# Performance work log

Hardware: AMD Instinct MI355X
Metric: run time of the kernel (lower is better)

Reference implementation:

```python
import jax, jax.numpy as jnp
import numpy as np

N = 64    # input_size (number of causal nodes)
H = 512   # hidden_size
M = 64    # mediate_size
B = 1024  # batched derivative evaluations (original processes one (1,N) state at a time)


def setup_inputs() -> dict:
    key = jax.random.key(0)
    ks = jax.random.split(key, 8)
    s = lambda fan_in: 1.0 / np.sqrt(fan_in)
    x = jax.random.normal(ks[0], (B, N), dtype=jnp.float32)
    # stacked per-node weights (one set per node i in 0..N-1)
    W1 = jax.random.uniform(ks[1], (N, H, N), jnp.float32, -s(N), s(N))        # net_1 layer 1, no bias
    W2 = jax.random.uniform(ks[2], (N, M, H), jnp.float32, -s(H), s(H))        # net_1 layer 2, no bias
    W3 = jax.random.uniform(ks[3], (N, H, M + N), jnp.float32, -s(M + N), s(M + N))  # net_3 layer 1
    b3 = jax.random.uniform(ks[4], (N, H), jnp.float32, -s(M + N), s(M + N))
    W4 = jax.random.uniform(ks[5], (N, H), jnp.float32, -s(H), s(H))           # net_3 layer 2 (out dim 1)
    b4 = jax.random.uniform(ks[6], (N,), jnp.float32, -s(H), s(H))
    return {"x": x, "W1": W1, "W2": W2, "W3": W3, "b3": b3, "W4": W4, "b4": b4}


def reference(x, W1, W2, W3, b3, W4, b4):
    # Faithful DAG-case CausalDerivative.forward, batched over B states and
    # grouped over the N per-node MLPs (replacing N python-loop iterations).
    eye = jnp.eye(N, dtype=x.dtype)
    inputs_1 = x[:, None, :] * (1.0 - eye)          # (B, N, N): node i sees all-but-own value
    inputs_2 = x[:, None, :] * eye                  # (B, N, N): node i sees only own value
    h1 = jax.nn.relu(jnp.einsum('bni,nhi->bnh', inputs_1, W1))   # (B, N, H)
    r1 = jax.nn.relu(jnp.einsum('bnh,nmh->bnm', h1, W2))         # (B, N, M)
    rep3 = jnp.concatenate([r1, inputs_2], axis=-1)              # (B, N, M+N)
    h3 = jax.nn.relu(jnp.einsum('bnk,nhk->bnh', rep3, W3) + b3)  # (B, N, H)
    out = jax.nn.relu(jnp.einsum('bnh,nh->bn', h3, W4) + b4)     # (B, N) derivatives
    return out
```

## Files before the change

kernel.cpp:

```cpp
#include <hip/hip_runtime.h>

#define NN 64
#define HH 512

typedef _Float16 h8 __attribute__((ext_vector_type(8)));
typedef float    fx4 __attribute__((ext_vector_type(4)));

#define MFMA __builtin_amdgcn_mfma_f32_16x16x32_f16

__device__ __forceinline__ void cvt_store16(_Float16* d, const float4* p) {
    h8 h0, h1;
    h0[0]=(_Float16)p[0].x; h0[1]=(_Float16)p[0].y; h0[2]=(_Float16)p[0].z; h0[3]=(_Float16)p[0].w;
    h0[4]=(_Float16)p[1].x; h0[5]=(_Float16)p[1].y; h0[6]=(_Float16)p[1].z; h0[7]=(_Float16)p[1].w;
    h1[0]=(_Float16)p[2].x; h1[1]=(_Float16)p[2].y; h1[2]=(_Float16)p[2].z; h1[3]=(_Float16)p[2].w;
    h1[4]=(_Float16)p[3].x; h1[5]=(_Float16)p[3].y; h1[6]=(_Float16)p[3].z; h1[7]=(_Float16)p[3].w;
    *(h8*)d = h0; *((h8*)d + 1) = h1;
}

__global__ __launch_bounds__(256, 2)
void causal_mfma3(const float* __restrict__ x,  const float* __restrict__ W1,
                  const float* __restrict__ W2, const float* __restrict__ W3,
                  const float* __restrict__ b3, const float* __restrict__ W4,
                  const float* __restrict__ b4, float* __restrict__ out)
{
    __shared__ __align__(16) char smem[61952];
    _Float16* W1c  = (_Float16*)smem;
    _Float16* W2c  = W1c + 2 * 4608;
    _Float16* priv = W2c + 2 * 4608;
    float*    w3cs = (float*)(smem + 55296);
    float*    b3s  = w3cs + 512;
    float*    w4s  = b3s + 512;
    float*    xns  = w4s + 512;

    const int tid  = threadIdx.x;
    const int bid  = blockIdx.x;
    const int n    = bid & 63;
    const int tile = bid >> 6;
    const int lane = tid & 63;
    const int pos  = lane & 15;
    const int quad = lane >> 4;
    const int wv   = __builtin_amdgcn_readfirstlane(tid >> 6);
    const int row0 = tile * 128;
    const int wrow = wv << 5;

    const float* W1n = W1 + (size_t)n * HH * NN;
    const float* W2n = W2 + (size_t)n * NN * HH;
    const float* W3n = W3 + (size_t)n * HH * 128;

    const int trow = tid >> 2;
    const int tcol = (tid & 3) << 4;

    {
        float4 p1[4], p2[4];
        #pragma unroll
        for (int q = 0; q < 4; ++q) p1[q] = *(const float4*)(W1n + trow * 64 + tcol + q * 4);
        #pragma unroll
        for (int q = 0; q < 4; ++q) p2[q] = *(const float4*)(W2n + (size_t)trow * HH + tcol + q * 4);
        #pragma unroll
        for (int k = 0; k < 2; ++k) {
            const int h = tid + k * 256;
            w3cs[h] = W3n[(size_t)h * 128 + 64 + n];
            b3s[h]  = b3[n * HH + h];
            w4s[h]  = W4[n * HH + h];
        }
        if (tid < 128) xns[tid] = x[(size_t)(row0 + tid) * NN + n];
        cvt_store16(W1c + trow * 72 + tcol, p1);
        cvt_store16(W2c + trow * 72 + tcol, p2);
    }

    h8 aX[2][2];
    #pragma unroll
    for (int mt = 0; mt < 2; ++mt)
        #pragma unroll
        for (int ks = 0; ks < 2; ++ks) {
            const float* p = x + (size_t)(row0 + wrow + mt * 16 + pos) * NN + ks * 32 + quad * 8;
            float4 a = *(const float4*)p, bq = *(const float4*)(p + 4);
            float v[8] = {a.x, a.y, a.z, a.w, bq.x, bq.y, bq.z, bq.w};
            const int base = ks * 32 + quad * 8;
            #pragma unroll
            for (int j = 0; j < 8; ++j) if (base + j == n) v[j] = 0.f;
            h8 h;
            #pragma unroll
            for (int j = 0; j < 8; ++j) h[j] = (_Float16)v[j];
            aX[mt][ks] = h;
        }
    __syncthreads();

    _Float16* P = priv + wv * 2304;

    fx4 acc2[2][4] = {};
    for (int c = 0; c < 8; ++c) {
        const int cb = c & 1;
        float4 p1[4], p2[4];
        if (c < 7) {
            const int hb1 = (c + 1) << 6;
            #pragma unroll
            for (int q = 0; q < 4; ++q) p1[q] = *(const float4*)(W1n + (hb1 + trow) * 64 + tcol + q * 4);
            #pragma unroll
            for (int q = 0; q < 4; ++q) p2[q] = *(const float4*)(W2n + (size_t)trow * HH + hb1 + tcol + q * 4);
        }
        const _Float16* W1L = W1c + cb * 4608;
        fx4 accA[2][4] = {};
        #pragma unroll
        for (int ks = 0; ks < 2; ++ks)
            #pragma unroll
            for (int nt = 0; nt < 4; ++nt) {
                h8 bf = *(const h8*)(W1L + (nt * 16 + pos) * 72 + ks * 32 + quad * 8);
                accA[0][nt] = MFMA(aX[0][ks], bf, accA[0][nt], 0, 0, 0);
                accA[1][nt] = MFMA(aX[1][ks], bf, accA[1][nt], 0, 0, 0);
            }
        #pragma unroll
        for (int mt = 0; mt < 2; ++mt)
            #pragma unroll
            for (int nt = 0; nt < 4; ++nt)
                #pragma unroll
                for (int r = 0; r < 4; ++r)
                    P[(mt * 16 + quad * 4 + r) * 72 + nt * 16 + pos] =
                        (_Float16)fmaxf(accA[mt][nt][r], 0.f);
        h8 aH[2][2];
        #pragma unroll
        for (int mt = 0; mt < 2; ++mt)
            #pragma unroll
            for (int ks = 0; ks < 2; ++ks)
                aH[mt][ks] = *(const h8*)(P + (mt * 16 + pos) * 72 + ks * 32 + quad * 8);
        const _Float16* W2L = W2c + cb * 4608;
        #pragma unroll
        for (int ks = 0; ks < 2; ++ks)
            #pragma unroll
            for (int cm = 0; cm < 4; ++cm) {
                h8 bf = *(const h8*)(W2L + (cm * 16 + pos) * 72 + ks * 32 + quad * 8);
                acc2[0][cm] = MFMA(aH[0][ks], bf, acc2[0][cm], 0, 0, 0);
                acc2[1][cm] = MFMA(aH[1][ks], bf, acc2[1][cm], 0, 0, 0);
            }
        if (c < 7) {
            cvt_store16(W1c + (cb ^ 1) * 4608 + trow * 72 + tcol, p1);
            cvt_store16(W2c + (cb ^ 1) * 4608 + trow * 72 + tcol, p2);
        }
        __syncthreads();
    }

    #pragma unroll
    for (int mt = 0; mt < 2; ++mt)
        #pragma unroll
        for (int cm = 0; cm < 4; ++cm)
            #pragma unroll
            for (int r = 0; r < 4; ++r)
                P[(mt * 16 + quad * 4 + r) * 72 + cm * 16 + pos] =
                    (_Float16)fmaxf(acc2[mt][cm][r], 0.f);
    h8 aR[2][2];
    #pragma unroll
    for (int mt = 0; mt < 2; ++mt)
        #pragma unroll
        for (int ks = 0; ks < 2; ++ks)
            aR[mt][ks] = *(const h8*)(P + (mt * 16 + pos) * 72 + ks * 32 + quad * 8);
    h8 af3[2];
    #pragma unroll
    for (int mt = 0; mt < 2; ++mt) {
        h8 h;
        #pragma unroll
        for (int j = 0; j < 8; ++j) h[j] = (_Float16)0.f;
        if (quad == 0) { h[0] = (_Float16)xns[wrow + mt * 16 + pos]; h[1] = (_Float16)1.f; }
        af3[mt] = h;
    }

    {
        float4 p3[4];
        #pragma unroll
        for (int q = 0; q < 4; ++q) p3[q] = *(const float4*)(W3n + (size_t)trow * 128 + tcol + q * 4);
        cvt_store16(W1c + trow * 72 + tcol, p3);
    }
    __syncthreads();

    float o[2][4] = {};
    for (int c = 0; c < 8; ++c) {
        const int cb = c & 1;
        const int hc = c << 6;
        float4 p3[4];
        if (c < 7) {
            #pragma unroll
            for (int q = 0; q < 4; ++q)
                p3[q] = *(const float4*)(W3n + (size_t)(hc + 64 + trow) * 128 + tcol + q * 4);
        }
        const _Float16* W3L = W1c + cb * 4608;
        fx4 acc3[2][4] = {};
        #pragma unroll
        for (int ks = 0; ks < 2; ++ks)
            #pragma unroll
            for (int nt = 0; nt < 4; ++nt) {
                h8 bf = *(const h8*)(W3L + (nt * 16 + pos) * 72 + ks * 32 + quad * 8);
                acc3[0][nt] = MFMA(aR[0][ks], bf, acc3[0][nt], 0, 0, 0);
                acc3[1][nt] = MFMA(aR[1][ks], bf, acc3[1][nt], 0, 0, 0);
            }
        #pragma unroll
        for (int nt = 0; nt < 4; ++nt) {
            h8 bf3;
            #pragma unroll
            for (int j = 0; j < 8; ++j) bf3[j] = (_Float16)0.f;
            if (quad == 0) {
                const int h = hc + nt * 16 + pos;
                bf3[0] = (_Float16)w3cs[h];
                bf3[1] = (_Float16)b3s[h];
            }
            acc3[0][nt] = MFMA(af3[0], bf3, acc3[0][nt], 0, 0, 0);
            acc3[1][nt] = MFMA(af3[1], bf3, acc3[1][nt], 0, 0, 0);
        }
        #pragma unroll
        for (int nt = 0; nt < 4; ++nt) {
            const float w4v = w4s[hc + nt * 16 + pos];
            #pragma unroll
            for (int mt = 0; mt < 2; ++mt)
                #pragma unroll
                for (int r = 0; r < 4; ++r)
                    o[mt][r] = fmaf(fmaxf(acc3[mt][nt][r], 0.f), w4v, o[mt][r]);
        }
        if (c < 7) cvt_store16(W1c + (cb ^ 1) * 4608 + trow * 72 + tcol, p3);
        __syncthreads();
    }

    #pragma unroll
    for (int m = 1; m < 16; m <<= 1)
        #pragma unroll
        for (int mt = 0; mt < 2; ++mt)
            #pragma unroll
            for (int r = 0; r < 4; ++r)
                o[mt][r] += __shfl_xor(o[mt][r], m, 64);

    if (pos == 0) {
        const float bb = b4[n];
        #pragma unroll
        for (int mt = 0; mt < 2; ++mt)
            #pragma unroll
            for (int r = 0; r < 4; ++r) {
                const int row = row0 + wrow + mt * 16 + quad * 4 + r;
                out[(size_t)row * 64 + n] = fmaxf(o[mt][r] + bb, 0.f);
            }
    }
}

extern "C" void kernel_launch(void* const* d_in, const int* in_sizes, int n_in,
                              void* d_out, int out_size, void* d_ws, size_t ws_size,
                              hipStream_t stream)
{
    const float* x  = (const float*)d_in[0];
    const float* W1 = (const float*)d_in[1];
    const float* W2 = (const float*)d_in[2];
    const float* W3 = (const float*)d_in[3];
    const float* b3 = (const float*)d_in[4];
    const float* W4 = (const float*)d_in[5];
    const float* b4 = (const float*)d_in[6];
    float* out = (float*)d_out;
    hipLaunchKernelGGL(causal_mfma3, dim3(512), dim3(256), 0, stream,
                       x, W1, W2, W3, b3, W4, b4, out);
}
```

Measured before the change: 112.7 us.

## Pre-convert weights to fp16 in workspace and read MFMA operands from global

Adds a separate kernel that converts W1, W2 and the first 64 columns of W3 to fp16 in the workspace once per call, and extracts the diagonal W3 column into fp32. The main kernel then reads MFMA B operands straight from global/L2 instead of staging converted weights in large shared memory, using much less LDS per block. The node-own input term and bias are folded into an extra MFMA. This is meant to remove repeated per-block fp32-to-fp16 conversion and LDS staging, at the cost of an extra launch and extra global traffic for the converted weights.

```diff
diff --git a/kernel.cpp b/kernel.cpp
--- a/kernel.cpp
+++ b/kernel.cpp
@@ -7,6 +7,227 @@
 typedef float    fx4 __attribute__((ext_vector_type(4)));
 
 #define MFMA __builtin_amdgcn_mfma_f32_16x16x32_f16
+
+#define WS_NEEDED 12713984ull
+
+__global__ __launch_bounds__(256)
+void cvt_wts(const float* __restrict__ W1, const float* __restrict__ W2,
+             const float* __restrict__ W3, char* __restrict__ ws)
+{
+    _Float16* o1 = (_Float16*)ws;
+    _Float16* o2 = o1 + 2097152;
+    _Float16* o3 = o2 + 2097152;
+    float*    oc = (float*)(ws + 12582912);
+    const int g = blockIdx.x * 256 + threadIdx.x;
+
+    {
+        const float* s = W1 + (size_t)g * 8;
+        float4 a = *(const float4*)s, b = *(const float4*)(s + 4);
+        h8 h;
+        h[0]=(_Float16)a.x; h[1]=(_Float16)a.y; h[2]=(_Float16)a.z; h[3]=(_Float16)a.w;
+        h[4]=(_Float16)b.x; h[5]=(_Float16)b.y; h[6]=(_Float16)b.z; h[7]=(_Float16)b.w;
+        *(h8*)(o1 + (size_t)g * 8) = h;
+    }
+    {
+        const float* s = W2 + (size_t)g * 8;
+        float4 a = *(const float4*)s, b = *(const float4*)(s + 4);
+        h8 h;
+        h[0]=(_Float16)a.x; h[1]=(_Float16)a.y; h[2]=(_Float16)a.z; h[3]=(_Float16)a.w;
+        h[4]=(_Float16)b.x; h[5]=(_Float16)b.y; h[6]=(_Float16)b.z; h[7]=(_Float16)b.w;
+        *(h8*)(o2 + (size_t)g * 8) = h;
+    }
+    {
+        const int n3 = g >> 12;
+        const int h3 = (g >> 3) & 511;
+        const int k3 = (g & 7) * 8;
+        const float* s = W3 + (size_t)n3 * 65536 + h3 * 128 + k3;
+        float4 a = *(const float4*)s, b = *(const float4*)(s + 4);
+        h8 h;
+        h[0]=(_Float16)a.x; h[1]=(_Float16)a.y; h[2]=(_Float16)a.z; h[3]=(_Float16)a.w;
+        h[4]=(_Float16)b.x; h[5]=(_Float16)b.y; h[6]=(_Float16)b.z; h[7]=(_Float16)b.w;
+        *(h8*)(o3 + (size_t)g * 8) = h;
+    }
+    if (g < 32768) {
+        const int n3 = g >> 9;
+        const int h3 = g & 511;
+        oc[g] = W3[(size_t)n3 * 65536 + (size_t)h3 * 128 + 64 + n3];
+    }
+}
+
+__global__ __launch_bounds__(256, 2)
+void causal_mfma4(const float* __restrict__ x, const char* __restrict__ ws,
+                  const float* __restrict__ b3, const float* __restrict__ W4,
+                  const float* __restrict__ b4, float* __restrict__ out)
+{
+    __shared__ __align__(16) char smem[25088];
+    _Float16* priv = (_Float16*)smem;
+    float*    w3cs = (float*)(smem + 18432);
+    float*    b3s  = w3cs + 512;
+    float*    w4s  = b3s + 512;
+    float*    xns  = w4s + 512;
+
+    const int tid  = threadIdx.x;
+    const int bid  = blockIdx.x;
+    const int n    = bid & 63;
+    const int tile = bid >> 6;
+    const int lane = tid & 63;
+    const int pos  = lane & 15;
+    const int quad = lane >> 4;
+    const int wv   = __builtin_amdgcn_readfirstlane(tid >> 6);
+    const int row0 = tile * 128;
+    const int wrow = wv << 5;
+
+    const _Float16* W1h  = (const _Float16*)ws + (size_t)n * 32768;
+    const _Float16* W2h  = (const _Float16*)ws + 2097152 + (size_t)n * 32768;
+    const _Float16* W3h  = (const _Float16*)ws + 4194304 + (size_t)n * 32768;
+    const float*    w3cp = (const float*)(ws + 12582912) + n * 512;
+
+    #pragma unroll
+    for (int k = 0; k < 2; ++k) {
+        const int h = tid + k * 256;
+        w3cs[h] = w3cp[h];
+        b3s[h]  = b3[n * HH + h];
+        w4s[h]  = W4[n * HH + h];
+    }
+    if (tid < 128) xns[tid] = x[(size_t)(row0 + tid) * NN + n];
+
+    h8 aX[2][2];
+    #pragma unroll
+    for (int mt = 0; mt < 2; ++mt)
+        #pragma unroll
+        for (int ks = 0; ks < 2; ++ks) {
+            const float* p = x + (size_t)(row0 + wrow + mt * 16 + pos) * NN + ks * 32 + quad * 8;
+            float4 a = *(const float4*)p, bq = *(const float4*)(p + 4);
+            float v[8] = {a.x, a.y, a.z, a.w, bq.x, bq.y, bq.z, bq.w};
+            const int base = ks * 32 + quad * 8;
+            #pragma unroll
+            for (int j = 0; j < 8; ++j) if (base + j == n) v[j] = 0.f;
+            h8 h;
+            #pragma unroll
+            for (int j = 0; j < 8; ++j) h[j] = (_Float16)v[j];
+            aX[mt][ks] = h;
+        }
+    __syncthreads();
+
+    _Float16* P = priv + wv * 2304;
+
+    fx4 acc2[2][4] = {};
+    #pragma unroll 2
+    for (int c = 0; c < 8; ++c) {
+        const int hc = c << 6;
+        fx4 accA[2][4] = {};
+        #pragma unroll
+        for (int ks = 0; ks < 2; ++ks)
+            #pragma unroll
+            for (int nt = 0; nt < 4; ++nt) {
+                h8 bf = *(const h8*)(W1h + (hc + nt * 16 + pos) * 64 + ks * 32 + quad * 8);
+                accA[0][nt] = MFMA(aX[0][ks], bf, accA[0][nt], 0, 0, 0);
+                accA[1][nt] = MFMA(aX[1][ks], bf, accA[1][nt], 0, 0, 0);
+            }
+        #pragma unroll
+        for (int mt = 0; mt < 2; ++mt)
+            #pragma unroll
+            for (int nt = 0; nt < 4; ++nt)
+                #pragma unroll
+                for (int r = 0; r < 4; ++r)
+                    P[(mt * 16 + quad * 4 + r) * 72 + nt * 16 + pos] =
+                        (_Float16)fmaxf(accA[mt][nt][r], 0.f);
+        h8 aH[2][2];
+        #pragma unroll
+        for (int mt = 0; mt < 2; ++mt)
+            #pragma unroll
+            for (int ks = 0; ks < 2; ++ks)
+                aH[mt][ks] = *(const h8*)(P + (mt * 16 + pos) * 72 + ks * 32 + quad * 8);
+        #pragma unroll
+        for (int ks = 0; ks < 2; ++ks)
+            #pragma unroll
+            for (int cm = 0; cm < 4; ++cm) {
+                h8 bf = *(const h8*)(W2h + (cm * 16 + pos) * 512 + hc + ks * 32 + quad * 8);
+                acc2[0][cm] = MFMA(aH[0][ks], bf, acc2[0][cm], 0, 0, 0);
+                acc2[1][cm] = MFMA(aH[1][ks], bf, acc2[1][cm], 0, 0, 0);
+            }
+    }
+
+    #pragma unroll
+    for (int mt = 0; mt < 2; ++mt)
+        #pragma unroll
+        for (int cm = 0; cm < 4; ++cm)
+            #pragma unroll
+            for (int r = 0; r < 4; ++r)
+                P[(mt * 16 + quad * 4 + r) * 72 + cm * 16 + pos] =
+                    (_Float16)fmaxf(acc2[mt][cm][r], 0.f);
+    h8 aR[2][2];
+    #pragma unroll
+    for (int mt = 0; mt < 2; ++mt)
+        #pragma unroll
+        for (int ks = 0; ks < 2; ++ks)
+            aR[mt][ks] = *(const h8*)(P + (mt * 16 + pos) * 72 + ks * 32 + quad * 8);
+    h8 af3[2];
+    #pragma unroll
+    for (int mt = 0; mt < 2; ++mt) {
+        h8 h;
+        #pragma unroll
+        for (int j = 0; j < 8; ++j) h[j] = (_Float16)0.f;
+        if (quad == 0) { h[0] = (_Float16)xns[wrow + mt * 16 + pos]; h[1] = (_Float16)1.f; }
+        af3[mt] = h;
+    }
+
+    float o[2][4] = {};
+    #pragma unroll 2
+    for (int c = 0; c < 8; ++c) {
+        const int hc = c << 6;
+        fx4 acc3[2][4] = {};
+        #pragma unroll
+        for (int ks = 0; ks < 2; ++ks)
+            #pragma unroll
+            for (int nt = 0; nt < 4; ++nt) {
+                h8 bf = *(const h8*)(W3h + (hc + nt * 16 + pos) * 64 + ks * 32 + quad * 8);
+                acc3[0][nt] = MFMA(aR[0][ks], bf, acc3[0][nt], 0, 0, 0);
+                acc3[1][nt] = MFMA(aR[1][ks], bf, acc3[1][nt], 0, 0, 0);
+            }
+        #pragma unroll
+        for (int nt = 0; nt < 4; ++nt) {
+            h8 bf3;
+            #pragma unroll
+            for (int j = 0; j < 8; ++j) bf3[j] = (_Float16)0.f;
+            if (quad == 0) {
+                const int h = hc + nt * 16 + pos;
+                bf3[0] = (_Float16)w3cs[h];
+                bf3[1] = (_Float16)b3s[h];
+            }
+            acc3[0][nt] = MFMA(af3[0], bf3, acc3[0][nt], 0, 0, 0);
+            acc3[1][nt] = MFMA(af3[1], bf3, acc3[1][nt], 0, 0, 0);
+        }
+        #pragma unroll
+        for (int nt = 0; nt < 4; ++nt) {
+            const float w4v = w4s[hc + nt * 16 + pos];
+            #pragma unroll
+            for (int mt = 0; mt < 2; ++mt)
+                #pragma unroll
+                for (int r = 0; r < 4; ++r)
+                    o[mt][r] = fmaf(fmaxf(acc3[mt][nt][r], 0.f), w4v, o[mt][r]);
+        }
+    }
+
+    #pragma unroll
+    for (int m = 1; m < 16; m <<= 1)
+        #pragma unroll
+        for (int mt = 0; mt < 2; ++mt)
+            #pragma unroll
+            for (int r = 0; r < 4; ++r)
+                o[mt][r] += __shfl_xor(o[mt][r], m, 64);
+
+    if (pos == 0) {
+        const float bb = b4[n];
+        #pragma unroll
+        for (int mt = 0; mt < 2; ++mt)
+            #pragma unroll
+            for (int r = 0; r < 4; ++r) {
+                const int row = row0 + wrow + mt * 16 + quad * 4 + r;
+                out[(size_t)row * 64 + n] = fmaxf(o[mt][r] + bb, 0.f);
+            }
+    }
+}
 
 __device__ __forceinline__ void cvt_store16(_Float16* d, const float4* p) {
     h8 h0, h1;
@@ -249,6 +470,14 @@
     const float* W4 = (const float*)d_in[5];
     const float* b4 = (const float*)d_in[6];
     float* out = (float*)d_out;
-    hipLaunchKernelGGL(causal_mfma3, dim3(512), dim3(256), 0, stream,
-                       x, W1, W2, W3, b3, W4, b4, out);
+
+    if (d_ws != nullptr && ws_size >= WS_NEEDED) {
+        hipLaunchKernelGGL(cvt_wts, dim3(1024), dim3(256), 0, stream,
+                           W1, W2, W3, (char*)d_ws);
+        hipLaunchKernelGGL(causal_mfma4, dim3(512), dim3(256), 0, stream,
+                           x, (const char*)d_ws, b3, W4, b4, out);
+    } else {
+        hipLaunchKernelGGL(causal_mfma3, dim3(512), dim3(256), 0, stream,
+                           x, W1, W2, W3, b3, W4, b4, out);
+    }
 }
```

After: 136.7 us. 1.21x slower.
